# Performance work log

Hardware: AMD Instinct MI355X
Metric: run time of the kernel (lower is better)

## Reference

```python
import jax, jax.numpy as jnp
import numpy as np

HID = 256
HEADS = 8
HEAD_DIM = HID // HEADS

def setup_inputs() -> dict:
    key = jax.random.key(0)
    ks = jax.random.split(key, 12)
    B, S = 2, 4096
    scale = 1.0 / np.sqrt(HID)
    inp = {
        "query": jax.random.normal(ks[0], (B, S, HID), jnp.float32),
        "key": jax.random.normal(ks[1], (B, S, HID), jnp.float32),
        "value": jax.random.normal(ks[2], (B, S, HID), jnp.float32),
        "mask": jax.random.randint(ks[3], (B, 1, S), 0, 2, jnp.int32),
        "Wq": jax.random.normal(ks[4], (HID, HID), jnp.float32) * scale,
        "bq": jnp.zeros((HID,), jnp.float32),
        "Wk": jax.random.normal(ks[5], (HID, HID), jnp.float32) * scale,
        "bk": jnp.zeros((HID,), jnp.float32),
        "Wv": jax.random.normal(ks[6], (HID, HID), jnp.float32) * scale,
        "bv": jnp.zeros((HID,), jnp.float32),
        "Wo": jax.random.normal(ks[7], (HID, HID), jnp.float32) * scale,
        "bo": jnp.zeros((HID,), jnp.float32),
    }
    return inp

def reference(query, key, value, mask, Wq, bq, Wk, bk, Wv, bv, Wo, bo):
    B, Sq, _ = query.shape
    Sk = key.shape[1]
    # QKV projections, split into heads: [B, H, S, Dh]
    q = (query @ Wq + bq).reshape(B, Sq, HEADS, HEAD_DIM).transpose(0, 2, 1, 3)
    k = (key @ Wk + bk).reshape(B, Sk, HEADS, HEAD_DIM).transpose(0, 2, 1, 3)
    v = (value @ Wv + bv).reshape(B, Sk, HEADS, HEAD_DIM).transpose(0, 2, 1, 3)
    scores = jnp.einsum('bhqd,bhkd->bhqk', q, k) / jnp.sqrt(jnp.float32(HEAD_DIM))
    # mask [B,1,Sk] -> unsqueeze head dim -> [B,1,1,Sk], masked_fill(mask==0, -inf)
    m = mask[:, None, :, :]
    scores = jnp.where(m == 0, -jnp.inf, scores)
    attn = jax.nn.softmax(scores, axis=-1)  # dropout p=0.0 -> identity
    weighted = jnp.einsum('bhqk,bhkd->bhqd', attn, v)
    weighted = weighted.transpose(0, 2, 1, 3).reshape(B, Sq, HID)
    return weighted @ Wo + bo
```

## Files before the change

### kernel.cpp

```cpp
#include <hip/hip_runtime.h>
#include <math.h>

#define HID   256
#define HEADS 8
#define DH    32
#define BATCH 2
#define SEQ   4096
#define NTOK  (BATCH*SEQ)

typedef float f32x4 __attribute__((ext_vector_type(4)));
typedef short s16x8 __attribute__((ext_vector_type(8)));
typedef short s16x4 __attribute__((ext_vector_type(4)));
typedef unsigned int u32x2 __attribute__((ext_vector_type(2)));

__device__ __forceinline__ unsigned short bf16_rne(float f) {
  unsigned u = __float_as_uint(f);
  unsigned r = u + 0x7fffu + ((u >> 16) & 1u);
  return (unsigned short)(r >> 16);
}

__device__ __forceinline__ float bf16_to_f32(unsigned short h) {
  return __uint_as_float(((unsigned)h) << 16);
}

__device__ __forceinline__ s16x8 cvt_bf16x8(f32x4 a, f32x4 b) {
  s16x8 t;
  t[0] = (short)bf16_rne(a[0]); t[1] = (short)bf16_rne(a[1]);
  t[2] = (short)bf16_rne(a[2]); t[3] = (short)bf16_rne(a[3]);
  t[4] = (short)bf16_rne(b[0]); t[5] = (short)bf16_rne(b[1]);
  t[6] = (short)bf16_rne(b[2]); t[7] = (short)bf16_rne(b[3]);
  return t;
}

__global__ __launch_bounds__(256) void prep_kernel(
    const float* __restrict__ Wq, const float* __restrict__ Wk,
    const float* __restrict__ Wv, const float* __restrict__ Wo,
    const int* __restrict__ mask,
    unsigned short* __restrict__ wT,
    unsigned short* __restrict__ mbf, float qscale)
{
  int id = blockIdx.x * 256 + threadIdx.x;
  if (id < 4 * 65536) {
    int w = id >> 16;
    int r = id & 65535;
    int n = r >> 8, k = r & 255;
    const float* W = (w == 0) ? Wq : (w == 1) ? Wk : (w == 2) ? Wv : Wo;
    float v = W[k * 256 + n];
    if (w == 0) v *= qscale;
    wT[id] = bf16_rne(v);
  } else if (id < 4 * 65536 + NTOK) {
    int i = id - 4 * 65536;
    mbf[i] = mask[i] ? (unsigned short)0x3F80 : (unsigned short)0;
  }
}

__global__ __launch_bounds__(256) void qkv_proj(
    const float* __restrict__ qin, const float* __restrict__ kin,
    const float* __restrict__ vin, const int* __restrict__ mask,
    const unsigned short* __restrict__ wT,
    const float* __restrict__ bq, const float* __restrict__ bk,
    const float* __restrict__ bv,
    unsigned short* __restrict__ q_ws, unsigned short* __restrict__ kh_ws,
    unsigned short* __restrict__ vt_ws, float qscale)
{
  __shared__ unsigned short As[2][64 * 40];
  __shared__ unsigned short Ws[2][64 * 40];

  const int z = blockIdx.z;
  const float* A = (z == 0) ? qin : (z == 1) ? kin : vin;
  const unsigned short* W = wT + z * 65536;
  const float* bias = (z == 0) ? bq : (z == 1) ? bk : bv;
  const float bscale = (z == 0) ? qscale : 1.f;

  const int tid = threadIdx.x;
  const int lane = tid & 63;
  const int wv = tid >> 6;
  const int l16 = lane & 15, q4 = lane >> 4;
  const int Mblk = blockIdx.x * 64, Nblk = blockIdx.y * 64;
  const int M0 = Mblk + (wv & 1) * 32;
  const int N0 = Nblk + (wv >> 1) * 32;

  const int srow = tid >> 2, scol = (tid & 3) * 8;
  const float* Aps = A + (size_t)(Mblk + srow) * 256 + scol;
  const unsigned short* Wps = W + (size_t)(Nblk + srow) * 256 + scol;
  unsigned short* adst = &As[0][srow * 40 + scol];
  unsigned short* wdst = &Ws[0][srow * 40 + scol];

  f32x4 areg0, areg1; s16x8 wreg;

#define LOADCH(K) do {                                                         \
    areg0 = *(const f32x4*)(Aps + (K) * 32);                                   \
    areg1 = *(const f32x4*)(Aps + (K) * 32 + 4);                               \
    wreg  = *(const s16x8*)(Wps + (K) * 32);                                   \
  } while (0)
#define WRITECH(B) do {                                                        \
    *(s16x8*)(adst + (B) * (64 * 40)) = cvt_bf16x8(areg0, areg1);              \
    *(s16x8*)(wdst + (B) * (64 * 40)) = wreg;                                  \
  } while (0)

  f32x4 acc[2][2] = {};

  LOADCH(0); WRITECH(0); LOADCH(1);
  for (int k = 0; k < 8; ++k) {
    __syncthreads();
    if (k + 1 < 8) WRITECH((k + 1) & 1);
    if (k + 2 < 8) LOADCH(k + 2);
    const unsigned short* AL = &As[k & 1][0];
    const unsigned short* WL = &Ws[k & 1][0];
    s16x8 af[2], wf[2];
#pragma unroll
    for (int i = 0; i < 2; ++i)
      af[i] = *(const s16x8*)(AL + ((wv & 1) * 32 + i * 16 + l16) * 40 + q4 * 8);
#pragma unroll
    for (int j = 0; j < 2; ++j)
      wf[j] = *(const s16x8*)(WL + ((wv >> 1) * 32 + j * 16 + l16) * 40 + q4 * 8);
#pragma unroll
    for (int i = 0; i < 2; ++i)
#pragma unroll
      for (int j = 0; j < 2; ++j)
        acc[i][j] = __builtin_amdgcn_mfma_f32_16x16x32_bf16(af[i], wf[j], acc[i][j], 0, 0, 0);
  }
#undef LOADCH
#undef WRITECH

#pragma unroll
  for (int j = 0; j < 2; ++j) {
    int n = N0 + j * 16 + l16;
    float bb = bias[n] * bscale;
#pragma unroll
    for (int i = 0; i < 2; ++i) {
      int m0 = M0 + i * 16 + q4 * 4;
      f32x4 c = acc[i][j];
      c[0] += bb; c[1] += bb; c[2] += bb; c[3] += bb;
      if (z == 0) {
#pragma unroll
        for (int r = 0; r < 4; ++r)
          q_ws[(size_t)(m0 + r) * 256 + n] = bf16_rne(c[r]);
      } else if (z == 1) {
        int bi = m0 >> 12, s = m0 & 4095;
        int h = n >> 5, d = n & 31;
        unsigned short* o = kh_ws + ((size_t)(bi * 8 + h) * 4096 + s) * 32 + d;
#pragma unroll
        for (int r = 0; r < 4; ++r) o[(size_t)r * 32] = bf16_rne(c[r]);
      } else {
#pragma unroll
        for (int r = 0; r < 4; ++r) c[r] *= (float)mask[m0 + r];
        int bi = m0 >> 12, s = m0 & 4095;
        int h = n >> 5, d = n & 31;
        int T = s >> 6, sl = s & 63;
        unsigned lo = (unsigned)bf16_rne(c[0]) | ((unsigned)bf16_rne(c[1]) << 16);
        unsigned hi = (unsigned)bf16_rne(c[2]) | ((unsigned)bf16_rne(c[3]) << 16);
        unsigned* dst = (unsigned*)(vt_ws +
            ((size_t)((bi * 8 + h) * 64 + T) * 32 + d) * 64 + sl);
        dst[0] = lo; dst[1] = hi;
      }
    }
  }
}

__global__ __launch_bounds__(256, 7) void flash_kernel(
    const unsigned short* __restrict__ q_ws, const unsigned short* __restrict__ kh_ws,
    const unsigned short* __restrict__ vt_ws, const unsigned short* __restrict__ mbf,
    unsigned short* __restrict__ pO, float* __restrict__ pL)
{
  __shared__ unsigned short Kb[2][64 * 40];
  __shared__ unsigned short Vb[2][32 * 72];

  const int idx = blockIdx.x;
  const int qt = idx & 31;
  const int kq = (idx >> 5) & 3;
  const int bh = idx >> 7;
  const int b = bh >> 3, h = bh & 7;
  const int tid = threadIdx.x;
  const int lane = tid & 63;
  const int wv = tid >> 6;
  const int l16 = lane & 15, q4 = lane >> 4;
  const int q0 = qt * 128 + wv * 32;

  s16x8 Qf[2];
#pragma unroll
  for (int qh = 0; qh < 2; ++qh)
    Qf[qh] = *(const s16x8*)(q_ws +
        (size_t)(b * 4096 + q0 + qh * 16 + l16) * 256 + h * 32 + q4 * 8);

  const unsigned short* Ksrc = kh_ws + ((size_t)bh * 4096 + kq * 1024) * 32;
  const unsigned short* Vsrc = vt_ws + (size_t)bh * 64 * 2048 + (size_t)kq * 16 * 2048;
  const unsigned short* Msrc = mbf + b * 4096 + kq * 1024 + q4 * 4;

  unsigned short* kdst = &Kb[0][(tid >> 2) * 40 + (tid & 3) * 8];
  unsigned short* vdst = &Vb[0][(tid >> 3) * 72 + (tid & 7) * 8];

  f32x4 o[2][2] = {{{0.f,0.f,0.f,0.f},{0.f,0.f,0.f,0.f}},
                   {{0.f,0.f,0.f,0.f},{0.f,0.f,0.f,0.f}}};
  f32x4 l[2] = {{0.f,0.f,0.f,0.f},{0.f,0.f,0.f,0.f}};

  const unsigned sel = (l16 == 0) ? 0xFFFFFFFFu : 0u;

  s16x8 kreg, vreg;

#define STAGE_LOAD(T) do {                                                     \
    kreg = *(const s16x8*)(Ksrc + (size_t)(T) * 2048 + tid * 8);               \
    vreg = *(const s16x8*)(Vsrc + (size_t)(T) * 2048 + tid * 8);               \
  } while (0)
#define STAGE_WRITE(B) do {                                                    \
    *(s16x8*)(kdst + (B) * (64 * 40)) = kreg;                                  \
    *(s16x8*)(vdst + (B) * (32 * 72)) = vreg;                                  \
  } while (0)

#define COMPUTE(B, T) do {                                                     \
    const unsigned short* KL = &Kb[B][0];                                      \
    const unsigned short* VL = &Vb[B][0];                                      \
    const f32x4 zz = {0.f, 0.f, 0.f, 0.f};                                     \
    s16x4 mreg[4];                                                             \
    _Pragma("unroll") for (int t = 0; t < 4; ++t)                              \
      mreg[t] = *(const s16x4*)(Msrc + (T) * 64 + t * 16);                     \
    _Pragma("unroll") for (int t = 0; t < 4; ++t) {                            \
      s16x8 kf = *(const s16x8*)(KL + (t * 16 + l16) * 40 + q4 * 8);           \
      f32x4 sc0 = __builtin_amdgcn_mfma_f32_16x16x32_bf16(kf, Qf[0], zz, 0, 0, 0); \
      f32x4 sc1 = __builtin_amdgcn_mfma_f32_16x16x32_bf16(kf, Qf[1], zz, 0, 0, 0); \
      unsigned a0 = __float_as_uint(__builtin_amdgcn_exp2f(sc0[0])) + 0x8000u; \
      unsigned a1 = __float_as_uint(__builtin_amdgcn_exp2f(sc0[1])) + 0x8000u; \
      unsigned a2 = __float_as_uint(__builtin_amdgcn_exp2f(sc0[2])) + 0x8000u; \
      unsigned a3 = __float_as_uint(__builtin_amdgcn_exp2f(sc0[3])) + 0x8000u; \
      unsigned c0 = __float_as_uint(__builtin_amdgcn_exp2f(sc1[0])) + 0x8000u; \
      unsigned c1 = __float_as_uint(__builtin_amdgcn_exp2f(sc1[1])) + 0x8000u; \
      unsigned c2 = __float_as_uint(__builtin_amdgcn_exp2f(sc1[2])) + 0x8000u; \
      unsigned c3 = __float_as_uint(__builtin_amdgcn_exp2f(sc1[3])) + 0x8000u; \
      u32x2 pk0, pk1;                                                          \
      pk0[0] = __builtin_amdgcn_perm(a1, a0, 0x07060302u);                     \
      pk0[1] = __builtin_amdgcn_perm(a3, a2, 0x07060302u);                     \
      pk1[0] = __builtin_amdgcn_perm(c1, c0, 0x07060302u);                     \
      pk1[1] = __builtin_amdgcn_perm(c3, c2, 0x07060302u);                     \
      s16x4 pf0 = __builtin_bit_cast(s16x4, pk0);                              \
      s16x4 pf1 = __builtin_bit_cast(s16x4, pk1);                              \
      u32x2 mm = __builtin_bit_cast(u32x2, mreg[t]);                           \
      mm[0] &= sel; mm[1] &= sel;                                              \
      s16x4 onesb = __builtin_bit_cast(s16x4, mm);                             \
      s16x4 vf0 = *(const s16x4*)(VL + l16 * 72 + t * 16 + q4 * 4);            \
      s16x4 vf1 = *(const s16x4*)(VL + (l16 + 16) * 72 + t * 16 + q4 * 4);     \
      o[0][0] = __builtin_amdgcn_mfma_f32_16x16x16bf16_1k(pf0, vf0, o[0][0], 0, 0, 0); \
      o[0][1] = __builtin_amdgcn_mfma_f32_16x16x16bf16_1k(pf0, vf1, o[0][1], 0, 0, 0); \
      o[1][0] = __builtin_amdgcn_mfma_f32_16x16x16bf16_1k(pf1, vf0, o[1][0], 0, 0, 0); \
      o[1][1] = __builtin_amdgcn_mfma_f32_16x16x16bf16_1k(pf1, vf1, o[1][1], 0, 0, 0); \
      l[0] = __builtin_amdgcn_mfma_f32_16x16x16bf16_1k(pf0, onesb, l[0], 0, 0, 0); \
      l[1] = __builtin_amdgcn_mfma_f32_16x16x16bf16_1k(pf1, onesb, l[1], 0, 0, 0); \
    }                                                                          \
  } while (0)

  STAGE_LOAD(0); STAGE_WRITE(0);
  STAGE_LOAD(1);

  for (int T = 0; T < 16; ++T) {
    __syncthreads();
    if (T + 1 < 16) STAGE_WRITE((T + 1) & 1);
    if (T + 2 < 16) STAGE_LOAD(T + 2);
    COMPUTE(T & 1, T);
  }
#undef STAGE_LOAD
#undef STAGE_WRITE
#undef COMPUTE

  unsigned short* pob = pO + (((size_t)kq * 16 + bh) * 4096 + q0) * 32;
#pragma unroll
  for (int qh = 0; qh < 2; ++qh)
#pragma unroll
    for (int r = 0; r < 4; ++r) {
      int q = qh * 16 + q4 * 4 + r;
      pob[(size_t)q * 32 + l16]      = bf16_rne(o[qh][0][r]);
      pob[(size_t)q * 32 + l16 + 16] = bf16_rne(o[qh][1][r]);
    }
  if (l16 == 0) {
    float* plb = pL + ((size_t)kq * 16 + bh) * 4096 + q0;
#pragma unroll
    for (int qh = 0; qh < 2; ++qh)
#pragma unroll
      for (int r = 0; r < 4; ++r)
        plb[qh * 16 + q4 * 4 + r] = l[qh][r];
  }
}

__global__ __launch_bounds__(256) void combine_kernel(
    const unsigned short* __restrict__ pO, const float* __restrict__ pL,
    unsigned short* __restrict__ wtd)
{
  int id = blockIdx.x * 256 + threadIdx.x;
  int d8 = id & 3;
  int q  = (id >> 2) & 4095;
  int bh = id >> 14;
  int b = bh >> 3, h = bh & 7;
  const size_t OS = (size_t)16 * 4096 * 32;
  const size_t LS = (size_t)16 * 4096;
  size_t i0 = ((size_t)bh * 4096 + q) * 32 + d8 * 8;

  float s[8] = {0.f,0.f,0.f,0.f,0.f,0.f,0.f,0.f};
  float lt = 0.f;
#pragma unroll
  for (int kq = 0; kq < 4; ++kq) {
    s16x8 v = *(const s16x8*)(pO + kq * OS + i0);
#pragma unroll
    for (int j = 0; j < 8; ++j) s[j] += bf16_to_f32((unsigned short)v[j]);
    lt += pL[kq * LS + (size_t)bh * 4096 + q];
  }
  float inv = 1.0f / lt;
  s16x8 outp;
#pragma unroll
  for (int j = 0; j < 8; ++j) outp[j] = (short)bf16_rne(s[j] * inv);
  *(s16x8*)(wtd + ((size_t)(b * 4096 + q) * 256) + h * 32 + d8 * 8) = outp;
}

__global__ __launch_bounds__(256) void o_proj(
    const unsigned short* __restrict__ wtd, const unsigned short* __restrict__ woT,
    const float* __restrict__ bo, float* __restrict__ out)
{
  const int lane = threadIdx.x & 63;
  const int wv = threadIdx.x >> 6;
  const int l16 = lane & 15, q4 = lane >> 4;
  const int M0 = blockIdx.x * 64 + (wv & 1) * 32;
  const int N0 = blockIdx.y * 64 + (wv >> 1) * 32;

  f32x4 acc[2][2] = {};
  for (int k0 = 0; k0 < 256; k0 += 32) {
    s16x8 af[2], wf[2];
#pragma unroll
    for (int i = 0; i < 2; ++i)
      af[i] = *(const s16x8*)(wtd + (size_t)(M0 + i * 16 + l16) * 256 + k0 + q4 * 8);
#pragma unroll
    for (int j = 0; j < 2; ++j)
      wf[j] = *(const s16x8*)(woT + (size_t)(N0 + j * 16 + l16) * 256 + k0 + q4 * 8);
#pragma unroll
    for (int i = 0; i < 2; ++i)
#pragma unroll
      for (int j = 0; j < 2; ++j)
        acc[i][j] = __builtin_amdgcn_mfma_f32_16x16x32_bf16(af[i], wf[j], acc[i][j], 0, 0, 0);
  }

#pragma unroll
  for (int j = 0; j < 2; ++j) {
    int n = N0 + j * 16 + l16;
    float bb = bo[n];
#pragma unroll
    for (int i = 0; i < 2; ++i) {
      int m0 = M0 + i * 16 + q4 * 4;
#pragma unroll
      for (int r = 0; r < 4; ++r)
        out[(size_t)(m0 + r) * 256 + n] = acc[i][j][r] + bb;
    }
  }
}

extern "C" void kernel_launch(void* const* d_in, const int* in_sizes, int n_in,
                              void* d_out, int out_size, void* d_ws, size_t ws_size,
                              hipStream_t stream) {
  const float* query = (const float*)d_in[0];
  const float* key   = (const float*)d_in[1];
  const float* value = (const float*)d_in[2];
  const int*   mask  = (const int*)d_in[3];
  const float* Wq = (const float*)d_in[4];
  const float* bq = (const float*)d_in[5];
  const float* Wk = (const float*)d_in[6];
  const float* bk = (const float*)d_in[7];
  const float* Wv = (const float*)d_in[8];
  const float* bv = (const float*)d_in[9];
  const float* Wo = (const float*)d_in[10];
  const float* bo = (const float*)d_in[11];
  float* out = (float*)d_out;

  char* p = (char*)d_ws;
  unsigned short* q_ws  = (unsigned short*)p; p += (size_t)NTOK * HID * 2;
  unsigned short* kh_ws = (unsigned short*)p; p += (size_t)NTOK * HID * 2;
  unsigned short* vt_ws = (unsigned short*)p; p += (size_t)NTOK * HID * 2;
  unsigned short* wtd   = (unsigned short*)p; p += (size_t)NTOK * HID * 2;
  unsigned short* wT    = (unsigned short*)p; p += (size_t)4 * 65536 * 2;
  unsigned short* mbf   = (unsigned short*)p; p += (size_t)NTOK * 2;
  unsigned short* pO    = (unsigned short*)p; p += (size_t)4 * 16 * 4096 * 32 * 2;
  float* pL             = (float*)p;          p += (size_t)4 * 16 * 4096 * 4;

  const float qscale = 1.0f / (sqrtf(32.0f) * logf(2.0f));

  prep_kernel<<<(4 * 65536 + NTOK + 255) / 256, 256, 0, stream>>>(
      Wq, Wk, Wv, Wo, mask, wT, mbf, qscale);
  qkv_proj<<<dim3(NTOK / 64, HID / 64, 3), 256, 0, stream>>>(
      query, key, value, mask, wT, bq, bk, bv, q_ws, kh_ws, vt_ws, qscale);
  flash_kernel<<<dim3(2048), 256, 0, stream>>>(
      q_ws, kh_ws, vt_ws, mbf, pO, pL);
  combine_kernel<<<dim3(1024), 256, 0, stream>>>(pO, pL, wtd);
  o_proj<<<dim3(NTOK / 64, HID / 64), 256, 0, stream>>>(
      wtd, wT + 3 * 65536, bo, out);
}
```

Baseline: 180.0 us.

## Fuse split-K combine into output projection with double-buffered LDS staging

Removes the separate combine kernel and the wtd intermediate buffer. The output projection now reads the four partial attention outputs and their softmax sums directly, normalizes them into bf16, and stages A and Wo tiles through double-buffered shared memory with register prefetch. This saves a kernel launch and a global write and read of the combined activations. In exchange, each of the 4 N-blocks recomputes the combine for its M tile, so partial outputs are read four times instead of once.

```diff
diff --git a/kernel.cpp b/kernel.cpp
--- a/kernel.cpp
+++ b/kernel.cpp
@@ -279,60 +279,83 @@
   }
 }
 
-__global__ __launch_bounds__(256) void combine_kernel(
+__global__ __launch_bounds__(256) void o_proj(
     const unsigned short* __restrict__ pO, const float* __restrict__ pL,
-    unsigned short* __restrict__ wtd)
+    const unsigned short* __restrict__ woT,
+    const float* __restrict__ bo, float* __restrict__ out)
 {
-  int id = blockIdx.x * 256 + threadIdx.x;
-  int d8 = id & 3;
-  int q  = (id >> 2) & 4095;
-  int bh = id >> 14;
-  int b = bh >> 3, h = bh & 7;
+  __shared__ unsigned short As[2][64 * 40];
+  __shared__ unsigned short Ws[2][64 * 40];
+
+  const int tid = threadIdx.x;
+  const int lane = tid & 63;
+  const int wv = tid >> 6;
+  const int l16 = lane & 15, q4 = lane >> 4;
+  const int Mblk = blockIdx.x * 64, Nblk = blockIdx.y * 64;
+  const int M0 = Mblk + (wv & 1) * 32;
+  const int N0 = Nblk + (wv >> 1) * 32;
+
+  const int srow = tid >> 2, scol = (tid & 3) * 8;
+  const int token = Mblk + srow;
+  const int b = token >> 12, s = token & 4095;
+  const unsigned short* Wps = woT + (size_t)(Nblk + srow) * 256 + scol;
+  unsigned short* adst = &As[0][srow * 40 + scol];
+  unsigned short* wdst = &Ws[0][srow * 40 + scol];
+
   const size_t OS = (size_t)16 * 4096 * 32;
   const size_t LS = (size_t)16 * 4096;
-  size_t i0 = ((size_t)bh * 4096 + q) * 32 + d8 * 8;
-
-  float s[8] = {0.f,0.f,0.f,0.f,0.f,0.f,0.f,0.f};
-  float lt = 0.f;
-#pragma unroll
-  for (int kq = 0; kq < 4; ++kq) {
-    s16x8 v = *(const s16x8*)(pO + kq * OS + i0);
-#pragma unroll
-    for (int j = 0; j < 8; ++j) s[j] += bf16_to_f32((unsigned short)v[j]);
-    lt += pL[kq * LS + (size_t)bh * 4096 + q];
-  }
-  float inv = 1.0f / lt;
-  s16x8 outp;
-#pragma unroll
-  for (int j = 0; j < 8; ++j) outp[j] = (short)bf16_rne(s[j] * inv);
-  *(s16x8*)(wtd + ((size_t)(b * 4096 + q) * 256) + h * 32 + d8 * 8) = outp;
-}
-
-__global__ __launch_bounds__(256) void o_proj(
-    const unsigned short* __restrict__ wtd, const unsigned short* __restrict__ woT,
-    const float* __restrict__ bo, float* __restrict__ out)
-{
-  const int lane = threadIdx.x & 63;
-  const int wv = threadIdx.x >> 6;
-  const int l16 = lane & 15, q4 = lane >> 4;
-  const int M0 = blockIdx.x * 64 + (wv & 1) * 32;
-  const int N0 = blockIdx.y * 64 + (wv >> 1) * 32;
+
+  s16x8 preg[4]; float lsum; s16x8 wreg;
+
+#define LOADCH(K) do {                                                         \
+    int _bh = b * 8 + (K);                                                     \
+    size_t _i0 = ((size_t)_bh * 4096 + s) * 32 + scol;                         \
+    preg[0] = *(const s16x8*)(pO + _i0);                                       \
+    preg[1] = *(const s16x8*)(pO + OS + _i0);                                  \
+    preg[2] = *(const s16x8*)(pO + 2 * OS + _i0);                              \
+    preg[3] = *(const s16x8*)(pO + 3 * OS + _i0);                              \
+    size_t _li = (size_t)_bh * 4096 + s;                                       \
+    lsum = pL[_li] + pL[LS + _li] + pL[2 * LS + _li] + pL[3 * LS + _li];       \
+    wreg = *(const s16x8*)(Wps + (K) * 32);                                    \
+  } while (0)
+#define WRITECH(B) do {                                                        \
+    float inv = 1.0f / lsum;                                                   \
+    s16x8 ap;                                                                  \
+    _Pragma("unroll") for (int j = 0; j < 8; ++j) {                            \
+      float v = bf16_to_f32((unsigned short)preg[0][j])                        \
+              + bf16_to_f32((unsigned short)preg[1][j])                        \
+              + bf16_to_f32((unsigned short)preg[2][j])                        \
+              + bf16_to_f32((unsigned short)preg[3][j]);                       \
+      ap[j] = (short)bf16_rne(v * inv);                                        \
+    }                                                                          \
+    *(s16x8*)(adst + (B) * (64 * 40)) = ap;                                    \
+    *(s16x8*)(wdst + (B) * (64 * 40)) = wreg;                                  \
+  } while (0)
 
   f32x4 acc[2][2] = {};
-  for (int k0 = 0; k0 < 256; k0 += 32) {
+
+  LOADCH(0); WRITECH(0); LOADCH(1);
+  for (int k = 0; k < 8; ++k) {
+    __syncthreads();
+    if (k + 1 < 8) WRITECH((k + 1) & 1);
+    if (k + 2 < 8) LOADCH(k + 2);
+    const unsigned short* AL = &As[k & 1][0];
+    const unsigned short* WL = &Ws[k & 1][0];
     s16x8 af[2], wf[2];
 #pragma unroll
     for (int i = 0; i < 2; ++i)
-      af[i] = *(const s16x8*)(wtd + (size_t)(M0 + i * 16 + l16) * 256 + k0 + q4 * 8);
+      af[i] = *(const s16x8*)(AL + ((wv & 1) * 32 + i * 16 + l16) * 40 + q4 * 8);
 #pragma unroll
     for (int j = 0; j < 2; ++j)
-      wf[j] = *(const s16x8*)(woT + (size_t)(N0 + j * 16 + l16) * 256 + k0 + q4 * 8);
+      wf[j] = *(const s16x8*)(WL + ((wv >> 1) * 32 + j * 16 + l16) * 40 + q4 * 8);
 #pragma unroll
     for (int i = 0; i < 2; ++i)
 #pragma unroll
       for (int j = 0; j < 2; ++j)
         acc[i][j] = __builtin_amdgcn_mfma_f32_16x16x32_bf16(af[i], wf[j], acc[i][j], 0, 0, 0);
   }
+#undef LOADCH
+#undef WRITECH
 
 #pragma unroll
   for (int j = 0; j < 2; ++j) {
@@ -369,7 +392,6 @@
   unsigned short* q_ws  = (unsigned short*)p; p += (size_t)NTOK * HID * 2;
   unsigned short* kh_ws = (unsigned short*)p; p += (size_t)NTOK * HID * 2;
   unsigned short* vt_ws = (unsigned short*)p; p += (size_t)NTOK * HID * 2;
-  unsigned short* wtd   = (unsigned short*)p; p += (size_t)NTOK * HID * 2;
   unsigned short* wT    = (unsigned short*)p; p += (size_t)4 * 65536 * 2;
   unsigned short* mbf   = (unsigned short*)p; p += (size_t)NTOK * 2;
   unsigned short* pO    = (unsigned short*)p; p += (size_t)4 * 16 * 4096 * 32 * 2;
@@ -383,7 +405,6 @@
       query, key, value, mask, wT, bq, bk, bv, q_ws, kh_ws, vt_ws, qscale);
   flash_kernel<<<dim3(2048), 256, 0, stream>>>(
       q_ws, kh_ws, vt_ws, mbf, pO, pL);
-  combine_kernel<<<dim3(1024), 256, 0, stream>>>(pO, pL, wtd);
   o_proj<<<dim3(NTOK / 64, HID / 64), 256, 0, stream>>>(
-      wtd, wT + 3 * 65536, bo, out);
-}
+      pO, pL, wT + 3 * 65536, bo, out);
+}
```

New measurement: 174.4 us. 1.03x faster.
